# Kernel optimization log

Hardware: AMD Instinct MI355X
Metric: run time of the kernel (lower is better)

## Reference

```python
import jax, jax.numpy as jnp
import numpy as np

ITERS = 10
SMOOTH = 1e-06


def _pool(x, wh, ww, ph, pw, is_max):
    # torch max_pool2d pads with -inf; min-pool (=-maxpool(-x)) thus pads with +inf.
    init = -jnp.inf if is_max else jnp.inf
    op = jax.lax.max if is_max else jax.lax.min
    return jax.lax.reduce_window(
        x, init, op,
        window_dimensions=(1, 1, wh, ww),
        window_strides=(1, 1, 1, 1),
        padding=((0, 0), (0, 0), (ph, ph), (pw, pw)))


def soft_erode(img):
    p1 = _pool(img, 3, 1, 1, 0, is_max=False)  # min over 3x1 window
    p2 = _pool(img, 1, 3, 0, 1, is_max=False)  # min over 1x3 window
    return jnp.minimum(p1, p2)


def soft_dilate(img):
    return _pool(img, 3, 3, 1, 1, is_max=True)


def soft_open(img):
    return soft_dilate(soft_erode(img))


def soft_skel(img, iters=ITERS):
    skel = jnp.zeros_like(img)
    for _ in range(iters):  # fixed small trip count; unrolled under jit
        opened = soft_open(img)
        skel = skel + jax.nn.relu(img - opened)
        img = soft_erode(img)
    return skel


def setup_inputs() -> dict:
    key = jax.random.key(0)
    k1, k2 = jax.random.split(key)
    B, C, H, W = 16, 1, 512, 512
    pred = jax.random.normal(k1, (B, C, H, W), dtype=jnp.float32)  # logits
    target = jax.random.randint(k2, (B, C, H, W), 0, 2).astype(jnp.float32)
    return {"pred": pred, "target": target}


def reference(pred, target):
    p = jax.nn.sigmoid(pred)
    skel_pred = soft_skel(p, ITERS)
    skel_gt = soft_skel(target.astype(jnp.float32), ITERS)
    tprec = jnp.sum(p * skel_gt) / (jnp.sum(skel_gt) + SMOOTH)
    tsens = jnp.sum(target * skel_pred) / (jnp.sum(skel_pred) + SMOOTH)
    cldice = 2.0 * tprec * tsens / (tprec + tsens + SMOOTH)
    return 1.0 - cldice
```

## Files before the change

kernel.cpp:

```cpp
#include <hip/hip_runtime.h>
#include <math.h>

#define HH 512
#define WW 512
#define NBATCH 16
#define RV 16
#define FSV (HH/RV)
#define FSH 5
#define NF (NBATCH*FSH*FSV)
#define BSU 13
#define BSV 4
#define NBT (NBATCH*BSU*BSV)
#define NTASK (NF + NBT)
#define NSTEP (RV + 23)
#define FINF  (__builtin_huge_valf())

__device__ __forceinline__ float sigf(float x) { return 1.0f / (1.0f + __expf(-x)); }
__device__ __forceinline__ float bperm(int a, float v) {
    return __int_as_float(__builtin_amdgcn_ds_bpermute(a, __float_as_int(v)));
}
__device__ __forceinline__ unsigned bpermu(int a, unsigned v) {
    return (unsigned)__builtin_amdgcn_ds_bpermute(a, (int)v);
}

template<bool GUARD>
__device__ __forceinline__ void do_strip(
    const float* __restrict__ ip, const float* __restrict__ wp,
    int r0, bool ok0, bool ok1, bool useX, bool useY,
    float mDx, float mDy, int aL, int aR,
    float* __restrict__ partials, int wid, int lane)
{
    float2 W[11][3], sk[10];
#pragma unroll
    for (int t = 0; t < 11; ++t)
#pragma unroll
        for (int j = 0; j < 3; ++j) W[t][j] = make_float2(FINF, FINF);
#pragma unroll
    for (int j = 0; j < 10; ++j) sk[j] = make_float2(0.f, 0.f);
    float2 wsum = make_float2(0.f, 0.f), rsum = make_float2(0.f, 0.f);

    for (int s = 0; s < NSTEP; ++s) {
        const int f = r0 - 11 + s;

        float2 nv;
        if (!GUARD || (f >= 0 && f < HH)) {
            float2 t0 = *(const float2*)(ip);
            float x = sigf(t0.x);
            float y = sigf(t0.y);
            nv.x = ok0 ? x : FINF;
            nv.y = ok1 ? y : FINF;
        } else { nv.x = FINF; nv.y = FINF; }
        ip += WW;

        if (s >= 14) {
#pragma unroll
            for (int j = 0; j < 9; ++j) sk[j] = sk[j + 1];
#pragma unroll
            for (int t = 0; t < 10; ++t) {
                float2 b0 = W[t + 1][0], b1 = W[t + 1][1], b2 = W[t + 1][2];
                if (GUARD) {
                    if (f - t - 4 < 0 || f - t - 4 >= HH) { b0.x = -FINF; b0.y = -FINF; }
                    if (f - t - 3 < 0 || f - t - 3 >= HH) { b1.x = -FINF; b1.y = -FINF; }
                    if (f - t - 2 < 0 || f - t - 2 >= HH) { b2.x = -FINF; b2.y = -FINF; }
                }
                float cmx = fmaxf(fmaxf(b0.x, b1.x), b2.x);
                float cmy = fmaxf(fmaxf(b0.y, b1.y), b2.y);
                cmx = fminf(cmx, mDx);
                cmy = fminf(cmy, mDy);
                float Lc = bperm(aL, cmy);
                float Rc = bperm(aR, cmx);
                float dx = fmaxf(fmaxf(cmx, Lc), cmy);
                float dy = fmaxf(fmaxf(cmy, cmx), Rc);
                float2 iq = W[t][0];
                float rx = fmaxf(iq.x - dx, 0.f);
                float ry = fmaxf(iq.y - dy, 0.f);
                rx = useX ? rx : 0.f;
                ry = useY ? ry : 0.f;
                if (t == 0) { sk[9].x = rx;       sk[9].y = ry; }
                else        { sk[9 - t].x += rx;  sk[9 - t].y += ry; }
            }
        }

        if (s >= 23) {
            float2 wv = *(const float2*)(wp);
            float wx = wv.x, wy = wv.y;
            wx = ok0 ? wx : 0.f;
            wy = ok1 ? wy : 0.f;
            wsum.x += wx * sk[0].x; wsum.y += wy * sk[0].y;
            rsum.x += sk[0].x;      rsum.y += sk[0].y;
            wp += WW;
        }

        float2 nr = nv;
#pragma unroll
        for (int t = 0; t < 10; ++t) {
            W[t][0] = W[t][1]; W[t][1] = W[t][2]; W[t][2] = nr;
            float2 a0 = W[t][0], a1 = W[t][1], a2 = W[t][2];
            if (GUARD) {
                if (f - t - 2 < 0 || f - t - 2 >= HH) { a0.x = FINF; a0.y = FINF; }
                if (f - t - 1 < 0 || f - t - 1 >= HH) { a1.x = FINF; a1.y = FINF; }
                if (f - t     < 0 || f - t     >= HH) { a2.x = FINF; a2.y = FINF; }
            }
            float mvx = fminf(fminf(a0.x, a1.x), a2.x);
            float mvy = fminf(fminf(a0.y, a1.y), a2.y);
            float Le = bperm(aL, a1.y);
            float Re = bperm(aR, a1.x);
            float ex = fminf(fminf(mvx, Le), a1.y);
            float ey = fminf(fminf(mvy, a1.x), Re);
            ex = fmaxf(ex, -mDx);
            ey = fmaxf(ey, -mDy);
            nr.x = ex; nr.y = ey;
        }
        W[10][0] = W[10][1]; W[10][1] = W[10][2]; W[10][2] = nr;
    }

    float pw = wsum.x + wsum.y;
    float pr = rsum.x + rsum.y;
#pragma unroll
    for (int off = 32; off; off >>= 1) {
        pw += __shfl_down(pw, off, 64);
        pr += __shfl_down(pr, off, 64);
    }
    if (lane == 0) { partials[2 * wid] = pw; partials[2 * wid + 1] = pr; }
}

__device__ void do_bits(const float* __restrict__ tgt, const float* __restrict__ prd,
                        int b, int u, int v, float* __restrict__ partials,
                        int wid, int lane)
{
    const int c = u * 40 - 12 + lane;
    const bool inImg = (c >= 0) && (c < WW);
    const int cc = min(max(c, 0), WW - 1);
    const size_t base = (size_t)b * HH * WW;
    const int w0 = 4 * v - 1;
    const int aL = ((lane + 63) & 63) << 2;
    const int aR = ((lane + 1) & 63) << 2;
    const bool vtop = (v == 0), vbot = (v == BSV - 1);

    unsigned w[6];
#pragma unroll
    for (int k = 0; k < 6; ++k) {
        const int gw = w0 + k;
        unsigned acc = 0xFFFFFFFFu;
        if (gw >= 0 && gw < 16) {
            acc = 0u;
            const float* rp = tgt + base + (size_t)(gw * 32) * WW + cc;
            for (int i = 0; i < 32; ++i) {
                acc |= ((__float_as_uint(*rp) >> 29) & 1u) << i;
                rp += WW;
            }
            acc = inImg ? acc : 0xFFFFFFFFu;
        }
        w[k] = acc;
    }

    unsigned P0[4] = {0,0,0,0}, P1[4] = {0,0,0,0}, P2[4] = {0,0,0,0}, P3[4] = {0,0,0,0};

#pragma unroll
    for (int t = 0; t < 10; ++t) {
        unsigned E[6];
#pragma unroll
        for (int k = 0; k < 6; ++k) {
            unsigned up = (w[k] << 1) | (k > 0 ? (w[k-1] >> 31) : 1u);
            unsigned dn = (w[k] >> 1) | (k < 5 ? (w[k+1] << 31) : 0x80000000u);
            unsigned vert = w[k] & up & dn;
            unsigned Lw = bpermu(aL, w[k]);
            unsigned Rw = bpermu(aR, w[k]);
            unsigned e = vert & Lw & Rw;
            E[k] = inImg ? e : 0xFFFFFFFFu;
        }
        if (vtop) E[0] = 0xFFFFFFFFu;
        if (vbot) E[5] = 0xFFFFFFFFu;

        const unsigned t0 = vtop ? 0u : E[0];
        const unsigned t5 = vbot ? 0u : E[5];
#pragma unroll
        for (int k = 1; k <= 4; ++k) {
            unsigned eu = (k == 1) ? t0 : E[k-1];
            unsigned ed = (k == 4) ? t5 : E[k+1];
            unsigned up = (E[k] << 1) | (eu >> 31);
            unsigned dn = (E[k] >> 1) | (ed << 31);
            unsigned V  = E[k] | up | dn;
            unsigned Vm = inImg ? V : 0u;
            unsigned D  = Vm | bpermu(aL, Vm) | bpermu(aR, Vm);
            unsigned contrib = w[k] & ~D;
            unsigned c0 = contrib & P0[k-1];  P0[k-1] ^= contrib;
            unsigned c1 = c0 & P1[k-1];       P1[k-1] ^= c0;
            unsigned c2 = c1 & P2[k-1];       P2[k-1] ^= c1;
            P3[k-1] ^= c2;
        }
#pragma unroll
        for (int k = 0; k < 6; ++k) w[k] = E[k];
    }

    const bool useful = inImg && (lane >= 12) && (lane < 52);
    unsigned rsum = 0;
#pragma unroll
    for (int k = 0; k < 4; ++k) {
        if (!useful) { P0[k] = 0; P1[k] = 0; P2[k] = 0; P3[k] = 0; }
        rsum += __popc(P0[k]) + 2*__popc(P1[k]) + 4*__popc(P2[k]) + 8*__popc(P3[k]);
    }
    float wsum = 0.f;
    const float* pp = prd + base + (size_t)(128 * v) * WW + cc;
    for (int i = 0; i < 32; ++i) {
#pragma unroll
        for (int k = 0; k < 4; ++k) {
            unsigned cnt = ((P0[k] >> i) & 1u) + (((P1[k] >> i) & 1u) << 1)
                         + (((P2[k] >> i) & 1u) << 2) + (((P3[k] >> i) & 1u) << 3);
            float p = sigf(pp[(size_t)(32 * k + i) * WW]);
            wsum += p * (float)cnt;
        }
    }

    float pw = wsum, pr = (float)rsum;
#pragma unroll
    for (int off = 32; off; off >>= 1) {
        pw += __shfl_down(pw, off, 64);
        pr += __shfl_down(pr, off, 64);
    }
    if (lane == 0) { partials[2 * wid] = pw; partials[2 * wid + 1] = pr; }
}

__global__ __launch_bounds__(256)
void cld_main(const float* __restrict__ pred, const float* __restrict__ target,
              float* __restrict__ partials)
{
    const int wid  = blockIdx.x * 4 + (threadIdx.x >> 6);
    const int lane = threadIdx.x & 63;

    if (wid < NF) {
        int t_ = wid;
        const int b = t_ / (FSH * FSV);  t_ -= b * (FSH * FSV);
        const int u = t_ / FSV;
        const int v = t_ - u * FSV;
        const int r0 = v * RV;
        const int cbase = u * 102 - 12;
        const int UW = (u == FSH - 1) ? 104 : 102;

        const int c0 = cbase + 2 * lane;
        const int c1 = c0 + 1;
        const bool ok0 = (c0 >= 0) && (c0 < WW);
        const bool ok1 = (c1 >= 0) && (c1 < WW);
        const int wc0 = 2 * lane;
        const bool useX = (wc0     >= 12) && (wc0     < 12 + UW);
        const bool useY = (wc0 + 1 >= 12) && (wc0 + 1 < 12 + UW);
        const float mDx = ok0 ? FINF : -FINF;
        const float mDy = ok1 ? FINF : -FINF;
        const int cc = min(max(c0, 0), WW - 2);
        const int aL = ((lane + 63) & 63) << 2;
        const int aR = ((lane + 1) & 63) << 2;

        const float* ip = pred   + (size_t)b * HH * WW + (ptrdiff_t)(r0 - 11) * WW + cc;
        const float* wp = target + (size_t)b * HH * WW + (size_t)r0 * WW + cc;

        if (v == 0 || v == FSV - 1)
            do_strip<true >(ip, wp, r0, ok0, ok1, useX, useY, mDx, mDy, aL, aR, partials, wid, lane);
        else
            do_strip<false>(ip, wp, r0, ok0, ok1, useX, useY, mDx, mDy, aL, aR, partials, wid, lane);
    } else {
        int idx = wid - NF;
        const int b = idx / (BSU * BSV);  idx -= b * (BSU * BSV);
        const int u = idx / BSV;
        const int v = idx - u * BSV;
        do_bits(target, pred, b, u, v, partials, wid, lane);
    }
}

__global__ void cld_final(const float* __restrict__ partials, float* __restrict__ out)
{
    const int tid = threadIdx.x;
    double a0 = 0, a1 = 0, a2 = 0, a3 = 0;
    for (int i = tid; i < NF; i += 256) {
        a0 += (double)partials[2 * i];
        a1 += (double)partials[2 * i + 1];
    }
    for (int i = NF + tid; i < NTASK; i += 256) {
        a2 += (double)partials[2 * i];
        a3 += (double)partials[2 * i + 1];
    }
    __shared__ double red[256][4];
    red[tid][0] = a0; red[tid][1] = a1; red[tid][2] = a2; red[tid][3] = a3;
    __syncthreads();
    for (int s2 = 128; s2 > 0; s2 >>= 1) {
        if (tid < s2) {
            red[tid][0] += red[tid + s2][0]; red[tid][1] += red[tid + s2][1];
            red[tid][2] += red[tid + s2][2]; red[tid][3] += red[tid + s2][3];
        }
        __syncthreads();
    }
    if (tid == 0) {
        double tsens = red[0][0] / (red[0][1] + 1e-6);
        double tprec = red[0][2] / (red[0][3] + 1e-6);
        double cl = 2.0 * tprec * tsens / (tprec + tsens + 1e-6);
        out[0] = (float)(1.0 - cl);
    }
}

extern "C" void kernel_launch(void* const* d_in, const int* in_sizes, int n_in,
                              void* d_out, int out_size, void* d_ws, size_t ws_size,
                              hipStream_t stream) {
    const float* pred   = (const float*)d_in[0];
    const float* target = (const float*)d_in[1];
    float* out = (float*)d_out;
    float* partials = (float*)d_ws;

    hipLaunchKernelGGL(cld_main, dim3(NTASK / 4), dim3(256), 0, stream,
                       pred, target, partials);
    hipLaunchKernelGGL(cld_final, dim3(1), dim3(256), 0, stream, partials, out);
}
```

Baseline: 77.51 us.

## Run soft-skeleton erosion/dilation stencil in packed fp16 with peeled loop phases

Converts the per-lane two-column sliding-window state for the predicted-probability skeleton from float2 to packed half2, so min/max ops become packed fp16 and each neighbor exchange needs one ds_bpermute per direction carrying both halves. The step loop is split into warm-up, steady and tail phases, so warm-up computes only the needed erosion levels and the per-step s>= branches go away. In the guarded variant the ALEVEL path drops the per-level row-boundary masking that the old code applied. fp16 storage of sigmoid values and residuals adds rounding error to the skeleton sums and the final loss.

```diff
diff --git a/kernel.cpp b/kernel.cpp
--- a/kernel.cpp
+++ b/kernel.cpp
@@ -12,110 +12,147 @@
 #define BSV 4
 #define NBT (NBATCH*BSU*BSV)
 #define NTASK (NF + NBT)
-#define NSTEP (RV + 23)
 #define FINF  (__builtin_huge_valf())
 
+typedef _Float16 h2 __attribute__((ext_vector_type(2)));
+
 __device__ __forceinline__ float sigf(float x) { return 1.0f / (1.0f + __expf(-x)); }
-__device__ __forceinline__ float bperm(int a, float v) {
-    return __int_as_float(__builtin_amdgcn_ds_bpermute(a, __float_as_int(v)));
-}
 __device__ __forceinline__ unsigned bpermu(int a, unsigned v) {
     return (unsigned)__builtin_amdgcn_ds_bpermute(a, (int)v);
+}
+__device__ __forceinline__ h2 h2bits(unsigned u) { return __builtin_bit_cast(h2, u); }
+__device__ __forceinline__ unsigned bitsh2(h2 h) { return __builtin_bit_cast(unsigned, h); }
+__device__ __forceinline__ h2 bperm2(int a, h2 v) { return h2bits(bpermu(a, bitsh2(v))); }
+__device__ __forceinline__ h2 hmin2(h2 a, h2 b) { return __builtin_elementwise_min(a, b); }
+__device__ __forceinline__ h2 hmax2(h2 a, h2 b) { return __builtin_elementwise_max(a, b); }
+__device__ __forceinline__ h2 lvec2(h2 prev, h2 self) {
+    return h2bits((bitsh2(prev) >> 16) | (bitsh2(self) << 16));
+}
+__device__ __forceinline__ h2 rvec2(h2 self, h2 next) {
+    return h2bits((bitsh2(self) >> 16) | (bitsh2(next) << 16));
 }
 
 template<bool GUARD>
 __device__ __forceinline__ void do_strip(
     const float* __restrict__ ip, const float* __restrict__ wp,
     int r0, bool ok0, bool ok1, bool useX, bool useY,
-    float mDx, float mDy, int aL, int aR,
+    h2 eclamp, h2 dclamp, int aL, int aR,
     float* __restrict__ partials, int wid, int lane)
 {
-    float2 W[11][3], sk[10];
-#pragma unroll
-    for (int t = 0; t < 11; ++t)
-#pragma unroll
-        for (int j = 0; j < 3; ++j) W[t][j] = make_float2(FINF, FINF);
-#pragma unroll
-    for (int j = 0; j < 10; ++j) sk[j] = make_float2(0.f, 0.f);
-    float2 wsum = make_float2(0.f, 0.f), rsum = make_float2(0.f, 0.f);
-
-    for (int s = 0; s < NSTEP; ++s) {
+    const h2 HP = h2bits(0x7C007C00u);
+    const h2 HN = h2bits(0xFC00FC00u);
+    const h2 HZ = h2bits(0u);
+
+    h2 W[11][3], sk[10];
+#pragma unroll
+    for (int t = 0; t < 11; ++t) { W[t][0] = HP; W[t][1] = HP; W[t][2] = HP; }
+#pragma unroll
+    for (int j = 0; j < 10; ++j) sk[j] = HZ;
+    float wsx = 0.f, wsy = 0.f, rsx = 0.f, rsy = 0.f;
+
+#define LOADROW(fv)                                                     \
+    h2 nv;                                                              \
+    {                                                                   \
+        if (!GUARD || (unsigned)(fv) < (unsigned)HH) {                  \
+            float2 t0 = *(const float2*)(ip);                           \
+            float x = sigf(t0.x); x = ok0 ? x : FINF;                   \
+            float y = sigf(t0.y); y = ok1 ? y : FINF;                   \
+            nv[0] = (_Float16)x; nv[1] = (_Float16)y;                   \
+        } else nv = HP;                                                 \
+        ip += WW;                                                       \
+    }
+
+#define ALEVEL(t)                                                       \
+    {                                                                   \
+        W[t][0] = W[t][1]; W[t][1] = W[t][2]; W[t][2] = nr;             \
+        h2 a0 = W[t][0], a1 = W[t][1], a2 = W[t][2];                    \
+        h2 vmin = hmin2(hmin2(a0, a1), a2);                             \
+        h2 pv = bperm2(aL, a1), nx = bperm2(aR, a1);                    \
+        h2 lv = lvec2(pv, a1), rv = rvec2(a1, nx);                      \
+        h2 e = hmin2(vmin, hmin2(lv, rv));                              \
+        nr = hmax2(e, eclamp);                                          \
+    }
+
+#define BLEVEL(t, fv)                                                   \
+    {                                                                   \
+        h2 b0 = W[t+1][0], b1 = W[t+1][1], b2 = W[t+1][2];              \
+        if (GUARD) {                                                    \
+            if ((unsigned)((fv) - t - 4) >= (unsigned)HH) b0 = HN;      \
+            if ((unsigned)((fv) - t - 3) >= (unsigned)HH) b1 = HN;      \
+            if ((unsigned)((fv) - t - 2) >= (unsigned)HH) b2 = HN;      \
+        }                                                               \
+        h2 cm = hmin2(hmax2(hmax2(b0, b1), b2), dclamp);                \
+        h2 pv = bperm2(aL, cm), nx = bperm2(aR, cm);                    \
+        h2 lv = lvec2(pv, cm), rv = rvec2(cm, nx);                      \
+        h2 d = hmax2(cm, hmax2(lv, rv));                                \
+        h2 df = hmax2(W[t][0] - d, HZ);                                 \
+        if (t == 0) sk[9] = df; else sk[9-t] = sk[9-t] + df;            \
+    }
+
+#define RINGSHIFT()                                                     \
+    {                                                                   \
+        _Pragma("unroll")                                               \
+        for (int j = 0; j < 9; ++j) sk[j] = sk[j + 1];                  \
+    }
+
+#define FINAL()                                                         \
+    {                                                                   \
+        float2 wv = *(const float2*)(wp); wp += WW;                     \
+        float c0v = (float)sk[0][0];                                    \
+        float c1v = (float)sk[0][1];                                    \
+        float cx = useX ? c0v : 0.f;                                    \
+        float cy = useY ? c1v : 0.f;                                    \
+        wsx += wv.x * cx; wsy += wv.y * cy;                             \
+        rsx += cx;        rsy += cy;                                    \
+    }
+
+    for (int s = 0; s < 14; ++s) {
         const int f = r0 - 11 + s;
-
-        float2 nv;
-        if (!GUARD || (f >= 0 && f < HH)) {
-            float2 t0 = *(const float2*)(ip);
-            float x = sigf(t0.x);
-            float y = sigf(t0.y);
-            nv.x = ok0 ? x : FINF;
-            nv.y = ok1 ? y : FINF;
-        } else { nv.x = FINF; nv.y = FINF; }
-        ip += WW;
-
-        if (s >= 14) {
-#pragma unroll
-            for (int j = 0; j < 9; ++j) sk[j] = sk[j + 1];
-#pragma unroll
-            for (int t = 0; t < 10; ++t) {
-                float2 b0 = W[t + 1][0], b1 = W[t + 1][1], b2 = W[t + 1][2];
-                if (GUARD) {
-                    if (f - t - 4 < 0 || f - t - 4 >= HH) { b0.x = -FINF; b0.y = -FINF; }
-                    if (f - t - 3 < 0 || f - t - 3 >= HH) { b1.x = -FINF; b1.y = -FINF; }
-                    if (f - t - 2 < 0 || f - t - 2 >= HH) { b2.x = -FINF; b2.y = -FINF; }
-                }
-                float cmx = fmaxf(fmaxf(b0.x, b1.x), b2.x);
-                float cmy = fmaxf(fmaxf(b0.y, b1.y), b2.y);
-                cmx = fminf(cmx, mDx);
-                cmy = fminf(cmy, mDy);
-                float Lc = bperm(aL, cmy);
-                float Rc = bperm(aR, cmx);
-                float dx = fmaxf(fmaxf(cmx, Lc), cmy);
-                float dy = fmaxf(fmaxf(cmy, cmx), Rc);
-                float2 iq = W[t][0];
-                float rx = fmaxf(iq.x - dx, 0.f);
-                float ry = fmaxf(iq.y - dy, 0.f);
-                rx = useX ? rx : 0.f;
-                ry = useY ? ry : 0.f;
-                if (t == 0) { sk[9].x = rx;       sk[9].y = ry; }
-                else        { sk[9 - t].x += rx;  sk[9 - t].y += ry; }
-            }
-        }
-
-        if (s >= 23) {
-            float2 wv = *(const float2*)(wp);
-            float wx = wv.x, wy = wv.y;
-            wx = ok0 ? wx : 0.f;
-            wy = ok1 ? wy : 0.f;
-            wsum.x += wx * sk[0].x; wsum.y += wy * sk[0].y;
-            rsum.x += sk[0].x;      rsum.y += sk[0].y;
-            wp += WW;
-        }
-
-        float2 nr = nv;
-#pragma unroll
-        for (int t = 0; t < 10; ++t) {
-            W[t][0] = W[t][1]; W[t][1] = W[t][2]; W[t][2] = nr;
-            float2 a0 = W[t][0], a1 = W[t][1], a2 = W[t][2];
-            if (GUARD) {
-                if (f - t - 2 < 0 || f - t - 2 >= HH) { a0.x = FINF; a0.y = FINF; }
-                if (f - t - 1 < 0 || f - t - 1 >= HH) { a1.x = FINF; a1.y = FINF; }
-                if (f - t     < 0 || f - t     >= HH) { a2.x = FINF; a2.y = FINF; }
-            }
-            float mvx = fminf(fminf(a0.x, a1.x), a2.x);
-            float mvy = fminf(fminf(a0.y, a1.y), a2.y);
-            float Le = bperm(aL, a1.y);
-            float Re = bperm(aR, a1.x);
-            float ex = fminf(fminf(mvx, Le), a1.y);
-            float ey = fminf(fminf(mvy, a1.x), Re);
-            ex = fmaxf(ex, -mDx);
-            ey = fmaxf(ey, -mDy);
-            nr.x = ex; nr.y = ey;
-        }
+        LOADROW(f);
+        h2 nr = nv;
+#pragma unroll
+        for (int t = 0; t < 6; ++t) ALEVEL(t);
+        W[6][0] = W[6][1]; W[6][1] = W[6][2]; W[6][2] = nr;
+    }
+    for (int s = 14; s < 23; ++s) {
+        const int f = r0 - 11 + s;
+        LOADROW(f);
+        RINGSHIFT();
+#pragma unroll
+        for (int t = 0; t < 10; ++t) BLEVEL(t, f);
+        h2 nr = nv;
+#pragma unroll
+        for (int t = 0; t < 10; ++t) ALEVEL(t);
         W[10][0] = W[10][1]; W[10][1] = W[10][2]; W[10][2] = nr;
     }
-
-    float pw = wsum.x + wsum.y;
-    float pr = rsum.x + rsum.y;
+    for (int s = 23; s < 38; ++s) {
+        const int f = r0 - 11 + s;
+        LOADROW(f);
+        RINGSHIFT();
+#pragma unroll
+        for (int t = 0; t < 10; ++t) BLEVEL(t, f);
+        FINAL();
+        h2 nr = nv;
+#pragma unroll
+        for (int t = 0; t < 10; ++t) ALEVEL(t);
+        W[10][0] = W[10][1]; W[10][1] = W[10][2]; W[10][2] = nr;
+    }
+    {
+        const int f = r0 - 11 + 38;
+        RINGSHIFT();
+#pragma unroll
+        for (int t = 0; t < 10; ++t) BLEVEL(t, f);
+        FINAL();
+    }
+
+#undef LOADROW
+#undef ALEVEL
+#undef BLEVEL
+#undef RINGSHIFT
+#undef FINAL
+
+    float pw = wsx + wsy;
+    float pr = rsx + rsy;
 #pragma unroll
     for (int off = 32; off; off >>= 1) {
         pw += __shfl_down(pw, off, 64);
@@ -244,8 +281,10 @@
         const int wc0 = 2 * lane;
         const bool useX = (wc0     >= 12) && (wc0     < 12 + UW);
         const bool useY = (wc0 + 1 >= 12) && (wc0 + 1 < 12 + UW);
-        const float mDx = ok0 ? FINF : -FINF;
-        const float mDy = ok1 ? FINF : -FINF;
+        const unsigned elo = ok0 ? 0xFC00u : 0x7C00u;
+        const unsigned ehi = ok1 ? 0xFC00u : 0x7C00u;
+        const h2 eclamp = h2bits(elo | (ehi << 16));
+        const h2 dclamp = h2bits((elo | (ehi << 16)) ^ 0x80008000u);
         const int cc = min(max(c0, 0), WW - 2);
         const int aL = ((lane + 63) & 63) << 2;
         const int aR = ((lane + 1) & 63) << 2;
@@ -254,9 +293,9 @@
         const float* wp = target + (size_t)b * HH * WW + (size_t)r0 * WW + cc;
 
         if (v == 0 || v == FSV - 1)
-            do_strip<true >(ip, wp, r0, ok0, ok1, useX, useY, mDx, mDy, aL, aR, partials, wid, lane);
+            do_strip<true >(ip, wp, r0, ok0, ok1, useX, useY, eclamp, dclamp, aL, aR, partials, wid, lane);
         else
-            do_strip<false>(ip, wp, r0, ok0, ok1, useX, useY, mDx, mDy, aL, aR, partials, wid, lane);
+            do_strip<false>(ip, wp, r0, ok0, ok1, useX, useY, eclamp, dclamp, aL, aR, partials, wid, lane);
     } else {
         int idx = wid - NF;
         const int b = idx / (BSU * BSV);  idx -= b * (BSU * BSV);
```

Result: slower. 83.76 us (+8.1%).
